# Performance work log

Measured on AMD Instinct MI355X. Metric: run time of the kernel, lower is better.

## Reference

```python
import jax, jax.numpy as jnp
import numpy as np

NH, NP = 8, 4  # n_heads, n_points
SHAPES = [(100, 167), (50, 84), (25, 42), (13, 21)]  # (H, W) per level


def setup_inputs() -> dict:
    key = jax.random.key(0)
    ks = jax.random.split(key, 8)
    bs, dm = 2, 256
    nl = len(SHAPES)
    nv = sum(h * w for h, w in SHAPES)  # 22223
    nq = nv
    s = 1.0 / np.sqrt(dm)
    return {
        'query': jax.random.normal(ks[0], (bs, nq, dm), jnp.float32),
        'value': jax.random.normal(ks[1], (bs, nv, dm), jnp.float32),
        'reference_points': jax.random.uniform(ks[2], (bs, nq, nl, 2), jnp.float32),
        'W_so': jax.random.normal(ks[3], (dm, NH * nl * NP * 2), jnp.float32) * 0.01,
        'b_so': jax.random.normal(ks[4], (NH * nl * NP * 2,), jnp.float32) * 0.5,
        'W_aw': jax.random.normal(ks[5], (dm, NH * nl * NP), jnp.float32) * s,
        'b_aw': jnp.zeros((NH * nl * NP,), jnp.float32),
        'W_vp': jax.random.normal(ks[6], (dm, dm), jnp.float32) * s,
        'b_vp': jnp.zeros((dm,), jnp.float32),
        'W_op': jax.random.normal(ks[7], (dm, dm), jnp.float32) * s,
        'b_op': jnp.zeros((dm,), jnp.float32),
        'spatial_shapes': jnp.array(SHAPES, jnp.int32),
    }


def _bilinear_gather(vf, H, W, loc):
    # vf: [BH, H*W, dh] flattened level feature map; loc: [BH, QP, 2] in [0,1]
    # Matches torch grid_sample(mode='bilinear', padding_mode='zeros', align_corners=False)
    x = loc[..., 0] * W - 0.5
    y = loc[..., 1] * H - 0.5
    x0f = jnp.floor(x); y0f = jnp.floor(y)
    lx = x - x0f; ly = y - y0f
    x0 = x0f.astype(jnp.int32); y0 = y0f.astype(jnp.int32)
    out = jnp.zeros(vf.shape[:1] + loc.shape[1:2] + vf.shape[-1:], vf.dtype)
    for dx, dy, w in ((0, 0, (1 - lx) * (1 - ly)), (1, 0, lx * (1 - ly)),
                      (0, 1, (1 - lx) * ly), (1, 1, lx * ly)):
        xi = x0 + dx; yi = y0 + dy
        valid = (xi >= 0) & (xi < W) & (yi >= 0) & (yi < H)
        idx = jnp.clip(yi, 0, H - 1) * W + jnp.clip(xi, 0, W - 1)  # [BH, QP]
        g = jnp.take_along_axis(vf, idx[:, :, None], axis=1)  # [BH, QP, dh]
        out = out + g * (w * valid)[:, :, None]
    return out


def _msda(value_heads, shapes_np, loc, aw):
    # value_heads: [bs,nv,nh,dh], loc: [bs,nq,nh,nl,np,2], aw: [bs,nq,nh,nl,np]
    bs, nv, nh, dh = value_heads.shape
    nq, nl, npnt = loc.shape[1], loc.shape[3], loc.shape[4]
    out = jnp.zeros((bs * nh, nq, dh), value_heads.dtype)
    start = 0
    for lvl in range(nl):
        H, W = int(shapes_np[lvl, 0]), int(shapes_np[lvl, 1])
        vf = value_heads[:, start:start + H * W].transpose(0, 2, 1, 3).reshape(bs * nh, H * W, dh)
        loc_l = loc[:, :, :, lvl].transpose(0, 2, 1, 3, 4).reshape(bs * nh, nq * npnt, 2)
        samp = _bilinear_gather(vf, H, W, loc_l).reshape(bs * nh, nq, npnt, dh)
        aw_l = aw[:, :, :, lvl].transpose(0, 2, 1, 3).reshape(bs * nh, nq, npnt)
        out = out + jnp.einsum('bqpd,bqp->bqd', samp, aw_l)
        start += H * W
    return out.reshape(bs, nh, nq, dh).transpose(0, 2, 1, 3).reshape(bs, nq, nh * dh)


def reference(query, value, reference_points, W_so, b_so, W_aw, b_aw, W_vp, b_vp, W_op, b_op, spatial_shapes):
    bs, nq, dm = query.shape
    nl = reference_points.shape[2]
    dh = dm // NH
    v = (value @ W_vp + b_vp).reshape(bs, value.shape[1], NH, dh)
    off = (query @ W_so + b_so).reshape(bs, nq, NH, nl, NP, 2)
    aw = jax.nn.softmax((query @ W_aw + b_aw).reshape(bs, nq, NH, nl * NP), axis=-1)
    aw = aw.reshape(bs, nq, NH, nl, NP)
    ss = np.asarray(spatial_shapes)  # static level metadata
    normalizer = jnp.asarray(np.stack([ss[:, 1], ss[:, 0]], -1), query.dtype)  # (w, h) per level
    loc = reference_points[:, :, None, :, None, :] + off / normalizer[None, None, None, :, None, :]
    out = _msda(v, ss, loc, aw)
    return out @ W_op + b_op + query  # identity residual (identity defaults to query)
```

## Files before the change

kernel.cpp:

```cpp
#include <hip/hip_runtime.h>
#include <hip/hip_bf16.h>
#include <math.h>

typedef __hip_bfloat16 bf16;
using f32x4  = __attribute__((ext_vector_type(4))) float;
using f32x2  = __attribute__((ext_vector_type(2))) float;
using bf16x8 = __attribute__((ext_vector_type(8))) short;
using f16x2  = __attribute__((ext_vector_type(2))) _Float16;

constexpr int BS = 2, NQ = 22223, MROWS = 44446;
constexpr int LH[4] = {100, 50, 25, 13};
constexpr int LW[4] = {167, 84, 42, 21};
constexpr int LSTART[4] = {0, 16700, 20900, 21950};
constexpr int PLW[4] = {170, 87, 45, 24};
constexpr int PLSTART[4] = {0, 17510, 22121, 23381};
constexpr int PTOT = 23765;

constexpr int BM = 128, BK = 32;
constexpr int LDT = 40;
constexpr int GX = (MROWS + BM - 1) / BM;

__global__ __launch_bounds__(256) void prep_weights(
    const float* __restrict__ W_vp, const float* __restrict__ W_so,
    const float* __restrict__ W_aw, const float* __restrict__ W_op,
    const float* __restrict__ b_so, const float* __restrict__ b_aw,
    bf16* __restrict__ Wt_vp, bf16* __restrict__ Wt_cat,
    bf16* __restrict__ Wt_op, float* __restrict__ bcat)
{
    int i = blockIdx.x * 256 + threadIdx.x;
    if (i < 256 * 256) {
        int n = i >> 8, k = i & 255;
        Wt_vp[i] = __float2bfloat16(W_vp[k * 256 + n]);
        Wt_op[i] = __float2bfloat16(W_op[k * 256 + n]);
    }
    if (i < 384 * 256) {
        int n = i >> 8, k = i & 255;
        float v = (n < 256) ? W_so[k * 256 + n] : W_aw[k * 128 + (n - 256)];
        Wt_cat[i] = __float2bfloat16(v);
    }
    if (i < 384) bcat[i] = (i < 256) ? b_so[i] : b_aw[i - 256];
}

__device__ inline int pad_base_idx(int pix) {
    if (pix < LSTART[1])      { int y = pix / 167;                  int x = pix - y * 167;                return PLSTART[0] + (y + 1) * 170 + (x + 1); }
    else if (pix < LSTART[2]) { int rel = pix - LSTART[1]; int y = rel / 84; int x = rel - y * 84;        return PLSTART[1] + (y + 1) * 87  + (x + 1); }
    else if (pix < LSTART[3]) { int rel = pix - LSTART[2]; int y = rel / 42; int x = rel - y * 42;        return PLSTART[2] + (y + 1) * 45  + (x + 1); }
    else                      { int rel = pix - LSTART[3]; int y = rel / 21; int x = rel - y * 21;        return PLSTART[3] + (y + 1) * 24  + (x + 1); }
}

template<bool A_BF16>
__device__ __forceinline__ void mfma_core(
    const void* __restrict__ Av, int lda, const bf16* __restrict__ Wt,
    int row0, int bn0, int M, bf16* As, bf16* Bs, f32x4 (&acc)[4][4])
{
    const int tid = threadIdx.x;
    const int lane = tid & 63;
    const int wv = tid >> 6;
    const int wm = (wv >> 1) * 64, wn = (wv & 1) * 64;
    const int l15 = lane & 15, l4 = lane >> 4;

#pragma unroll
    for (int m = 0; m < 4; ++m)
#pragma unroll
        for (int n = 0; n < 4; ++n) { acc[m][n][0]=0.f; acc[m][n][1]=0.f; acc[m][n][2]=0.f; acc[m][n][3]=0.f; }

    for (int k0 = 0; k0 < 256; k0 += BK) {
        __syncthreads();
#pragma unroll
        for (int t = 0; t < 2; ++t) {
            int idx = tid + t * 256;
            int r = idx >> 2, s = idx & 3;
            {
                int grow = row0 + r; if (grow >= M) grow = M - 1;
                bf16 tmp[8];
                if constexpr (A_BF16) {
                    const bf16* ap = (const bf16*)Av + (size_t)grow * lda + (k0 + s * 8);
                    *(uint4*)tmp = *(const uint4*)ap;
                } else {
                    const float* ap = (const float*)Av + (size_t)grow * lda + (k0 + s * 8);
                    f32x4 v0 = *(const f32x4*)ap;
                    f32x4 v1 = *(const f32x4*)(ap + 4);
#pragma unroll
                    for (int j = 0; j < 4; ++j) tmp[j] = __float2bfloat16(v0[j]);
#pragma unroll
                    for (int j = 0; j < 4; ++j) tmp[4 + j] = __float2bfloat16(v1[j]);
                }
                *(uint4*)&As[r * LDT + s * 8] = *(const uint4*)tmp;
            }
            *(uint4*)&Bs[r * LDT + s * 8] =
                *(const uint4*)(Wt + (size_t)(bn0 + r) * 256 + (k0 + s * 8));
        }
        __syncthreads();

        bf16x8 af[4], bfr[4];
#pragma unroll
        for (int m = 0; m < 4; ++m)
            af[m] = *(const bf16x8*)&As[(wm + m * 16 + l15) * LDT + l4 * 8];
#pragma unroll
        for (int n = 0; n < 4; ++n)
            bfr[n] = *(const bf16x8*)&Bs[(wn + n * 16 + l15) * LDT + l4 * 8];
#pragma unroll
        for (int m = 0; m < 4; ++m)
#pragma unroll
            for (int n = 0; n < 4; ++n)
                acc[m][n] = __builtin_amdgcn_mfma_f32_16x16x32_bf16(af[m], bfr[n], acc[m][n], 0, 0, 0);
    }
}

__global__ __launch_bounds__(256) void gemm_producer(
    const float* __restrict__ query, const float* __restrict__ value,
    const bf16* __restrict__ Wt_cat, const bf16* __restrict__ Wt_vp,
    const float* __restrict__ bcat, const float* __restrict__ bvp,
    bf16* __restrict__ offawl, _Float16* __restrict__ vproj)
{
    __shared__ bf16 As[BM * LDT];
    __shared__ bf16 Bs[BM * LDT];

    constexpr int NWG = GX * 5;
    constexpr int QXW = NWG / 8, RXW = NWG % 8;
    int orig = blockIdx.x;
    int xcd = orig & 7, seq = orig >> 3;
    int swz = (xcd < RXW ? xcd * (QXW + 1) : RXW * (QXW + 1) + (xcd - RXW) * QXW) + seq;
    int slice = swz % 5;
    int row0 = (swz / 5) * BM;

    const bool isOff = slice < 3;
    const void* A = isOff ? (const void*)query : (const void*)value;
    const bf16* Wt = isOff ? Wt_cat : Wt_vp;
    const float* bias = isOff ? bcat : bvp;
    int bn0 = isOff ? slice * 128 : (slice - 3) * 128;

    f32x4 acc[4][4];
    mfma_core<false>(A, 256, Wt, row0, bn0, MROWS, As, Bs, acc);

    const int lane = threadIdx.x & 63;
    const int wv = threadIdx.x >> 6;
    const int wm = (wv >> 1) * 64, wn = (wv & 1) * 64;
    const int l15 = lane & 15, l4 = lane >> 4;

    if (isOff) {
#pragma unroll
        for (int m = 0; m < 4; ++m)
#pragma unroll
            for (int j = 0; j < 4; ++j) {
                int r = row0 + wm + m * 16 + l4 * 4 + j;
                if (r < MROWS) {
                    bf16* orow = offawl + (size_t)r * 384;
#pragma unroll
                    for (int n = 0; n < 4; ++n) {
                        int fcol = bn0 + wn + n * 16 + l15;
                        orow[fcol] = __float2bfloat16(acc[m][n][j] + bias[fcol]);
                    }
                }
            }
    } else {
#pragma unroll
        for (int m = 0; m < 4; ++m)
#pragma unroll
            for (int j = 0; j < 4; ++j) {
                int r = row0 + wm + m * 16 + l4 * 4 + j;
                if (r < MROWS) {
                    int bb = (r >= NQ) ? 1 : 0;
                    int pb = pad_base_idx(r - bb * NQ);
#pragma unroll
                    for (int n = 0; n < 4; ++n) {
                        int fcol = bn0 + wn + n * 16 + l15;
                        int hh = fcol >> 5, cc = fcol & 31;
                        vproj[((size_t)(hh * 2 + bb) * PTOT + pb) * 32 + cc] =
                            (_Float16)(acc[m][n][j] + bias[fcol]);
                    }
                }
            }
    }
}

__global__ __launch_bounds__(256) void gemm_out(
    const bf16* __restrict__ msda, const bf16* __restrict__ Wt_op,
    const float* __restrict__ b_op, const float* __restrict__ query,
    float* __restrict__ out)
{
    __shared__ bf16 As[BM * LDT];
    __shared__ bf16 Bs[BM * LDT];

    constexpr int NWG = GX * 2;
    int orig = blockIdx.x;
    int swz = (orig & 7) * (NWG / 8) + (orig >> 3);
    int bn0 = (swz & 1) * 128;
    int row0 = (swz >> 1) * BM;

    f32x4 acc[4][4];
    mfma_core<true>(msda, 384, Wt_op, row0, bn0, MROWS, As, Bs, acc);

    const int lane = threadIdx.x & 63;
    const int wv = threadIdx.x >> 6;
    const int wm = (wv >> 1) * 64, wn = (wv & 1) * 64;
    const int l15 = lane & 15, l4 = lane >> 4;

#pragma unroll
    for (int m = 0; m < 4; ++m)
#pragma unroll
        for (int j = 0; j < 4; ++j) {
            int r = row0 + wm + m * 16 + l4 * 4 + j;
            if (r < MROWS) {
#pragma unroll
                for (int n = 0; n < 4; ++n) {
                    int fcol = bn0 + wn + n * 16 + l15;
                    out[(size_t)r * 256 + fcol] =
                        acc[m][n][j] + b_op[fcol] + query[(size_t)r * 256 + fcol];
                }
            }
        }
}

__device__ inline f32x2 bfpair(unsigned u) {
    f32x2 r;
    r.x = __uint_as_float(u << 16);
    r.y = __uint_as_float(u & 0xffff0000u);
    return r;
}

__global__ __launch_bounds__(256)
__attribute__((amdgpu_waves_per_eu(2, 4)))
void msda_sample18(
    const _Float16* __restrict__ vproj,
    const bf16* __restrict__ offawl,
    const float* __restrict__ refp,
    bf16* __restrict__ msda_out)
{
    __shared__ uint2 sOff[32][8];
    __shared__ uint2 sAwl[32][4];
    __shared__ float sRef[32][8];

    const int tid = threadIdx.x;
    const int head = blockIdx.x & 7;
    const int qbase = (blockIdx.x >> 3) * 32;

    {
        int row = tid >> 3, e = tid & 7;
        int grow = min(qbase + row, MROWS - 1);
        sOff[row][e] = *((const uint2*)(offawl + (size_t)grow * 384 + head * 32) + e);
        sRef[row][e] = refp[(size_t)grow * 8 + e];
        if (tid < 128) {
            int rowa = tid >> 2, ea = tid & 3;
            int growa = min(qbase + rowa, MROWS - 1);
            sAwl[rowa][ea] = *((const uint2*)(offawl + (size_t)growa * 384 + 256 + head * 16) + ea);
        }
    }
    __syncthreads();

    const int w = tid >> 6;
    const int lane = tid & 63;
    const int ql = lane >> 3;
    const int s = lane & 7;
    const int sx = s >> 2;
    const int c16 = s & 3;
    const int lq = w * 8 + ql;
    int q = qbase + lq;
    const bool alive = q < MROWS;
    if (!alive) q = MROWS - 1;
    const int b = (q >= NQ) ? 1 : 0;

    float aw0, aw1;
    {
        unsigned lgu = ((const unsigned*)&sAwl[lq][0])[s];
        f32x2 lg = bfpair(lgu);
        float m = fmaxf(lg.x, lg.y);
        m = fmaxf(m, __shfl_xor(m, 1));
        m = fmaxf(m, __shfl_xor(m, 2));
        m = fmaxf(m, __shfl_xor(m, 4));
        float e0 = __expf(lg.x - m), e1 = __expf(lg.y - m);
        float ssum = e0 + e1;
        ssum += __shfl_xor(ssum, 1);
        ssum += __shfl_xor(ssum, 2);
        ssum += __shfl_xor(ssum, 4);
        float inv = 1.f / ssum;
        aw0 = e0 * inv;
        aw1 = e1 * inv;
    }

    int rpix0, rpix1;
    int rw00, rw10, rw01, rw11;
    {
        const int lo = s >> 1;
        const int Wl  = (lo == 0) ? 167 : (lo == 1) ? 84 : (lo == 2) ? 42 : 21;
        const int Hl  = (lo == 0) ? 100 : (lo == 1) ? 50 : (lo == 2) ? 25 : 13;
        const int Wpl = (lo == 0) ? 170 : (lo == 1) ? 87 : (lo == 2) ? 45 : 24;
        const float xb = sRef[lq][lo * 2 + 0] * (float)Wl + 0.5f;
        const float yb = sRef[lq][lo * 2 + 1] * (float)Hl + 0.5f;
        uint2 ou = sOff[lq][s];
        unsigned ouv[2] = {ou.x, ou.y};
        float awv[2] = {aw0, aw1};
        int pixv[2]; int w0v[2], w1v[2];
#pragma unroll
        for (int k = 0; k < 2; ++k) {
            f32x2 o2 = bfpair(ouv[k]);
            float x = fminf(fmaxf(xb + o2.x, 0.f), (float)(Wl + 1));
            float y = fminf(fmaxf(yb + o2.y, 0.f), (float)(Hl + 1));
            float x0f = floorf(x), y0f = floorf(y);
            float lx = x - x0f, ly = y - y0f;
            float a = awv[k];
            float wy0 = (1.f - ly) * a, wy1 = ly * a;
            float wx0 = 1.f - lx;
            pixv[k] = ((int)y0f * Wpl + (int)x0f) * 32;
            w0v[k] = (int)__builtin_bit_cast(unsigned,
                        f16x2{(_Float16)(wx0 * wy0), (_Float16)(wx0 * wy1)});
            w1v[k] = (int)__builtin_bit_cast(unsigned,
                        f16x2{(_Float16)(lx * wy0), (_Float16)(lx * wy1)});
        }
        rpix0 = pixv[0]; rw00 = w0v[0]; rw10 = w1v[0];
        rpix1 = pixv[1]; rw01 = w0v[1]; rw11 = w1v[1];
    }

    const int srcbase = lane & 56;
    f16x2 acc0 = {0, 0}, acc1 = {0, 0}, acc2 = {0, 0}, acc3 = {0, 0};

#pragma unroll
    for (int l = 0; l < 4; ++l) {
        const int Wp = PLW[l];
        const _Float16* vl = vproj + ((size_t)(head * 2 + b) * PTOT + PLSTART[l]) * 32
                             + sx * 32 + c16 * 8;

        const _Float16* pr[4][2];
        f16x2 hw0[4], hw1[4];
#pragma unroll
        for (int p = 0; p < 4; ++p) {
            const int t = l * 4 + p;
            const int src = srcbase | (t >> 1);
            int pix, wa, wb;
            if (t & 1) {
                pix = __shfl(rpix1, src);
                wa  = __shfl(rw01, src);
                wb  = __shfl(rw11, src);
            } else {
                pix = __shfl(rpix0, src);
                wa  = __shfl(rw00, src);
                wb  = __shfl(rw10, src);
            }
            f16x2 wv = __builtin_bit_cast(f16x2, (unsigned)(sx ? wb : wa));
            hw0[p] = f16x2{wv[0], wv[0]};
            hw1[p] = f16x2{wv[1], wv[1]};
            pr[p][0] = vl + pix;
            pr[p][1] = pr[p][0] + Wp * 32;
        }

        uint4 c[4][2];
#pragma unroll
        for (int p = 0; p < 4; ++p) {
            c[p][0] = *(const uint4*)pr[p][0];
            c[p][1] = *(const uint4*)pr[p][1];
        }

#pragma unroll
        for (int p = 0; p < 4; ++p) {
            acc0 += __builtin_bit_cast(f16x2, c[p][0].x) * hw0[p];
            acc1 += __builtin_bit_cast(f16x2, c[p][0].y) * hw0[p];
            acc2 += __builtin_bit_cast(f16x2, c[p][0].z) * hw0[p];
            acc3 += __builtin_bit_cast(f16x2, c[p][0].w) * hw0[p];
            acc0 += __builtin_bit_cast(f16x2, c[p][1].x) * hw1[p];
            acc1 += __builtin_bit_cast(f16x2, c[p][1].y) * hw1[p];
            acc2 += __builtin_bit_cast(f16x2, c[p][1].z) * hw1[p];
            acc3 += __builtin_bit_cast(f16x2, c[p][1].w) * hw1[p];
        }
    }

    {
        unsigned u0 = __builtin_bit_cast(unsigned, acc0);
        unsigned u1 = __builtin_bit_cast(unsigned, acc1);
        unsigned u2 = __builtin_bit_cast(unsigned, acc2);
        unsigned u3 = __builtin_bit_cast(unsigned, acc3);
        acc0 += __builtin_bit_cast(f16x2, __shfl_xor((int)u0, 4));
        acc1 += __builtin_bit_cast(f16x2, __shfl_xor((int)u1, 4));
        acc2 += __builtin_bit_cast(f16x2, __shfl_xor((int)u2, 4));
        acc3 += __builtin_bit_cast(f16x2, __shfl_xor((int)u3, 4));
    }

    if (alive && sx == 0) {
        bf16 ob[8];
        ob[0] = __float2bfloat16((float)acc0[0]);
        ob[1] = __float2bfloat16((float)acc0[1]);
        ob[2] = __float2bfloat16((float)acc1[0]);
        ob[3] = __float2bfloat16((float)acc1[1]);
        ob[4] = __float2bfloat16((float)acc2[0]);
        ob[5] = __float2bfloat16((float)acc2[1]);
        ob[6] = __float2bfloat16((float)acc3[0]);
        ob[7] = __float2bfloat16((float)acc3[1]);
        *(uint4*)(msda_out + (size_t)q * 384 + head * 32 + c16 * 8) = *(const uint4*)ob;
    }
}

extern "C" void kernel_launch(void* const* d_in, const int* in_sizes, int n_in,
                              void* d_out, int out_size, void* d_ws, size_t ws_size,
                              hipStream_t stream) {
    const float* query = (const float*)d_in[0];
    const float* value = (const float*)d_in[1];
    const float* refp  = (const float*)d_in[2];
    const float* W_so  = (const float*)d_in[3];
    const float* b_so  = (const float*)d_in[4];
    const float* W_aw  = (const float*)d_in[5];
    const float* b_aw  = (const float*)d_in[6];
    const float* W_vp  = (const float*)d_in[7];
    const float* b_vp  = (const float*)d_in[8];
    const float* W_op  = (const float*)d_in[9];
    const float* b_op  = (const float*)d_in[10];
    float* out = (float*)d_out;

    bf16*     d_offawl = (bf16*)d_ws;
    _Float16* d_vproj  = (_Float16*)(d_offawl + (size_t)MROWS * 384);
    bf16*     d_wtcat  = (bf16*)(d_vproj + (size_t)16 * PTOT * 32);
    bf16*     d_wtvp   = d_wtcat + 384 * 256;
    bf16*     d_wtop   = d_wtvp + 256 * 256;
    float*    d_bcat   = (float*)(d_wtop + 256 * 256);

    prep_weights<<<384, 256, 0, stream>>>(W_vp, W_so, W_aw, W_op, b_so, b_aw,
                                          d_wtvp, d_wtcat, d_wtop, d_bcat);
    hipMemsetAsync(d_vproj, 0, (size_t)16 * PTOT * 32 * sizeof(_Float16), stream);

    gemm_producer<<<GX * 5, 256, 0, stream>>>(
        query, value, d_wtcat, d_wtvp, d_bcat, b_vp, d_offawl, d_vproj);

    msda_sample18<<<8 * ((MROWS + 31) / 32), 256, 0, stream>>>(
        d_vproj, d_offawl, refp, d_offawl);

    gemm_out<<<GX * 2, 256, 0, stream>>>(d_offawl, d_wtop, b_op, query, out);
}
```

Before: 138.4 us.

## Load GEMM operands directly from global into registers, dropping LDS staging

Both GEMM kernels stop staging A and B tiles through shared memory with barriers. Each wave now loads its MFMA fragments straight from global memory, and the K loop is fully unrolled. This removes the LDS round trip and the __syncthreads calls, and lets loads be issued ahead of the MFMAs. The cost is that data shared between waves is no longer reused in LDS, so global and L2 traffic per workgroup roughly doubles, and the fully unrolled loop raises register pressure.

```diff
diff --git a/kernel.cpp b/kernel.cpp
--- a/kernel.cpp
+++ b/kernel.cpp
@@ -16,8 +16,7 @@
 constexpr int PLSTART[4] = {0, 17510, 22121, 23381};
 constexpr int PTOT = 23765;
 
-constexpr int BM = 128, BK = 32;
-constexpr int LDT = 40;
+constexpr int BM = 128;
 constexpr int GX = (MROWS + BM - 1) / BM;
 
 __global__ __launch_bounds__(256) void prep_weights(
@@ -49,56 +48,55 @@
 }
 
 template<bool A_BF16>
-__device__ __forceinline__ void mfma_core(
+__device__ __forceinline__ void mfma_direct(
     const void* __restrict__ Av, int lda, const bf16* __restrict__ Wt,
-    int row0, int bn0, int M, bf16* As, bf16* Bs, f32x4 (&acc)[4][4])
+    int row0, int bn0, int M, f32x4 (&acc)[4][4])
 {
-    const int tid = threadIdx.x;
-    const int lane = tid & 63;
-    const int wv = tid >> 6;
+    const int lane = threadIdx.x & 63;
+    const int wv = threadIdx.x >> 6;
     const int wm = (wv >> 1) * 64, wn = (wv & 1) * 64;
     const int l15 = lane & 15, l4 = lane >> 4;
 
+    int arow[4];
+#pragma unroll
+    for (int m = 0; m < 4; ++m) {
+        int r = row0 + wm + m * 16 + l15;
+        arow[m] = (r < M) ? r : (M - 1);
+    }
+    const bf16* brow[4];
+#pragma unroll
+    for (int n = 0; n < 4; ++n)
+        brow[n] = Wt + (size_t)(bn0 + wn + n * 16 + l15) * 256 + l4 * 8;
+
 #pragma unroll
     for (int m = 0; m < 4; ++m)
 #pragma unroll
         for (int n = 0; n < 4; ++n) { acc[m][n][0]=0.f; acc[m][n][1]=0.f; acc[m][n][2]=0.f; acc[m][n][3]=0.f; }
 
-    for (int k0 = 0; k0 < 256; k0 += BK) {
-        __syncthreads();
-#pragma unroll
-        for (int t = 0; t < 2; ++t) {
-            int idx = tid + t * 256;
-            int r = idx >> 2, s = idx & 3;
-            {
-                int grow = row0 + r; if (grow >= M) grow = M - 1;
+#pragma unroll
+    for (int k0 = 0; k0 < 256; k0 += 32) {
+        bf16x8 af[4], bfr[4];
+#pragma unroll
+        for (int m = 0; m < 4; ++m) {
+            if constexpr (A_BF16) {
+                const bf16* ap = (const bf16*)Av + (size_t)arow[m] * lda + k0 + l4 * 8;
+                af[m] = *(const bf16x8*)ap;
+            } else {
+                const float* ap = (const float*)Av + (size_t)arow[m] * lda + k0 + l4 * 8;
+                f32x4 v0 = *(const f32x4*)ap;
+                f32x4 v1 = *(const f32x4*)(ap + 4);
                 bf16 tmp[8];
-                if constexpr (A_BF16) {
-                    const bf16* ap = (const bf16*)Av + (size_t)grow * lda + (k0 + s * 8);
-                    *(uint4*)tmp = *(const uint4*)ap;
-                } else {
-                    const float* ap = (const float*)Av + (size_t)grow * lda + (k0 + s * 8);
-                    f32x4 v0 = *(const f32x4*)ap;
-                    f32x4 v1 = *(const f32x4*)(ap + 4);
-#pragma unroll
-                    for (int j = 0; j < 4; ++j) tmp[j] = __float2bfloat16(v0[j]);
-#pragma unroll
-                    for (int j = 0; j < 4; ++j) tmp[4 + j] = __float2bfloat16(v1[j]);
-                }
-                *(uint4*)&As[r * LDT + s * 8] = *(const uint4*)tmp;
+#pragma unroll
+                for (int j = 0; j < 4; ++j) tmp[j] = __float2bfloat16(v0[j]);
+#pragma unroll
+                for (int j = 0; j < 4; ++j) tmp[4 + j] = __float2bfloat16(v1[j]);
+                af[m] = *(const bf16x8*)tmp;
             }
-            *(uint4*)&Bs[r * LDT + s * 8] =
-                *(const uint4*)(Wt + (size_t)(bn0 + r) * 256 + (k0 + s * 8));
-        }
-        __syncthreads();
-
-        bf16x8 af[4], bfr[4];
-#pragma unroll
-        for (int m = 0; m < 4; ++m)
-            af[m] = *(const bf16x8*)&As[(wm + m * 16 + l15) * LDT + l4 * 8];
+        }
 #pragma unroll
         for (int n = 0; n < 4; ++n)
-            bfr[n] = *(const bf16x8*)&Bs[(wn + n * 16 + l15) * LDT + l4 * 8];
+            bfr[n] = *(const bf16x8*)(brow[n] + k0);
+
 #pragma unroll
         for (int m = 0; m < 4; ++m)
 #pragma unroll
@@ -113,9 +111,6 @@
     const float* __restrict__ bcat, const float* __restrict__ bvp,
     bf16* __restrict__ offawl, _Float16* __restrict__ vproj)
 {
-    __shared__ bf16 As[BM * LDT];
-    __shared__ bf16 Bs[BM * LDT];
-
     constexpr int NWG = GX * 5;
     constexpr int QXW = NWG / 8, RXW = NWG % 8;
     int orig = blockIdx.x;
@@ -131,7 +126,7 @@
     int bn0 = isOff ? slice * 128 : (slice - 3) * 128;
 
     f32x4 acc[4][4];
-    mfma_core<false>(A, 256, Wt, row0, bn0, MROWS, As, Bs, acc);
+    mfma_direct<false>(A, 256, Wt, row0, bn0, MROWS, acc);
 
     const int lane = threadIdx.x & 63;
     const int wv = threadIdx.x >> 6;
@@ -179,9 +174,6 @@
     const float* __restrict__ b_op, const float* __restrict__ query,
     float* __restrict__ out)
 {
-    __shared__ bf16 As[BM * LDT];
-    __shared__ bf16 Bs[BM * LDT];
-
     constexpr int NWG = GX * 2;
     int orig = blockIdx.x;
     int swz = (orig & 7) * (NWG / 8) + (orig >> 3);
@@ -189,7 +181,7 @@
     int row0 = (swz >> 1) * BM;
 
     f32x4 acc[4][4];
-    mfma_core<true>(msda, 384, Wt_op, row0, bn0, MROWS, As, Bs, acc);
+    mfma_direct<true>(msda, 384, Wt_op, row0, bn0, MROWS, acc);
 
     const int lane = threadIdx.x & 63;
     const int wv = threadIdx.x >> 6;
```

New measurement: 204.0 us. 47.4% more time.

## Double-buffer LDS tiles and prefetch next K-slice in GEMM core

Applied to the files above, without the earlier changes.

Replaces the single-buffered GEMM main loop with a double-buffered version. The next K-slice of A and B is loaded from global memory into registers before the current slice's MFMAs run, then written to the alternate LDS buffer. This removes one barrier per iteration and hides global load latency behind compute. In exchange it doubles LDS use per block and adds register pressure, which can lower occupancy.

```diff
diff --git a/kernel.cpp b/kernel.cpp
--- a/kernel.cpp
+++ b/kernel.cpp
@@ -16,7 +16,7 @@
 constexpr int PLSTART[4] = {0, 17510, 22121, 23381};
 constexpr int PTOT = 23765;
 
-constexpr int BM = 128, BK = 32;
+constexpr int BM = 128;
 constexpr int LDT = 40;
 constexpr int GX = (MROWS + BM - 1) / BM;
 
@@ -49,7 +49,7 @@
 }
 
 template<bool A_BF16>
-__device__ __forceinline__ void mfma_core(
+__device__ __forceinline__ void mfma_core_db(
     const void* __restrict__ Av, int lda, const bf16* __restrict__ Wt,
     int row0, int bn0, int M, bf16* As, bf16* Bs, f32x4 (&acc)[4][4])
 {
@@ -59,51 +59,69 @@
     const int wm = (wv >> 1) * 64, wn = (wv & 1) * 64;
     const int l15 = lane & 15, l4 = lane >> 4;
 
+    const int sr0 = tid >> 2;
+    const int sr1 = sr0 + 64;
+    const int ss = tid & 3;
+    const int ga0 = min(row0 + sr0, M - 1);
+    const int ga1 = min(row0 + sr1, M - 1);
+
 #pragma unroll
     for (int m = 0; m < 4; ++m)
 #pragma unroll
         for (int n = 0; n < 4; ++n) { acc[m][n][0]=0.f; acc[m][n][1]=0.f; acc[m][n][2]=0.f; acc[m][n][3]=0.f; }
 
-    for (int k0 = 0; k0 < 256; k0 += BK) {
+    bf16 tA0[8], tA1[8];
+    uint4 tB0, tB1;
+
+    auto load_regs = [&](int k0) {
+        if constexpr (A_BF16) {
+            *(uint4*)tA0 = *(const uint4*)((const bf16*)Av + (size_t)ga0 * lda + k0 + ss * 8);
+            *(uint4*)tA1 = *(const uint4*)((const bf16*)Av + (size_t)ga1 * lda + k0 + ss * 8);
+        } else {
+            const float* ap0 = (const float*)Av + (size_t)ga0 * lda + k0 + ss * 8;
+            const float* ap1 = (const float*)Av + (size_t)ga1 * lda + k0 + ss * 8;
+            f32x4 v0 = *(const f32x4*)ap0, v1 = *(const f32x4*)(ap0 + 4);
+            f32x4 u0 = *(const f32x4*)ap1, u1 = *(const f32x4*)(ap1 + 4);
+#pragma unroll
+            for (int j = 0; j < 4; ++j) { tA0[j] = __float2bfloat16(v0[j]); tA0[4+j] = __float2bfloat16(v1[j]); }
+#pragma unroll
+            for (int j = 0; j < 4; ++j) { tA1[j] = __float2bfloat16(u0[j]); tA1[4+j] = __float2bfloat16(u1[j]); }
+        }
+        tB0 = *(const uint4*)(Wt + (size_t)(bn0 + sr0) * 256 + k0 + ss * 8);
+        tB1 = *(const uint4*)(Wt + (size_t)(bn0 + sr1) * 256 + k0 + ss * 8);
+    };
+    auto write_lds = [&](bf16* A_, bf16* B_) {
+        *(uint4*)&A_[sr0 * LDT + ss * 8] = *(const uint4*)tA0;
+        *(uint4*)&A_[sr1 * LDT + ss * 8] = *(const uint4*)tA1;
+        *(uint4*)&B_[sr0 * LDT + ss * 8] = tB0;
+        *(uint4*)&B_[sr1 * LDT + ss * 8] = tB1;
+    };
+
+    load_regs(0);
+    write_lds(As, Bs);
+    bf16 *curA = As, *curB = Bs;
+    bf16 *nxtA = As + BM * LDT, *nxtB = Bs + BM * LDT;
+
+#pragma unroll
+    for (int k = 0; k < 8; ++k) {
+        if (k < 7) load_regs((k + 1) * 32);
         __syncthreads();
-#pragma unroll
-        for (int t = 0; t < 2; ++t) {
-            int idx = tid + t * 256;
-            int r = idx >> 2, s = idx & 3;
-            {
-                int grow = row0 + r; if (grow >= M) grow = M - 1;
-                bf16 tmp[8];
-                if constexpr (A_BF16) {
-                    const bf16* ap = (const bf16*)Av + (size_t)grow * lda + (k0 + s * 8);
-                    *(uint4*)tmp = *(const uint4*)ap;
-                } else {
-                    const float* ap = (const float*)Av + (size_t)grow * lda + (k0 + s * 8);
-                    f32x4 v0 = *(const f32x4*)ap;
-                    f32x4 v1 = *(const f32x4*)(ap + 4);
-#pragma unroll
-                    for (int j = 0; j < 4; ++j) tmp[j] = __float2bfloat16(v0[j]);
-#pragma unroll
-                    for (int j = 0; j < 4; ++j) tmp[4 + j] = __float2bfloat16(v1[j]);
-                }
-                *(uint4*)&As[r * LDT + s * 8] = *(const uint4*)tmp;
-            }
-            *(uint4*)&Bs[r * LDT + s * 8] =
-                *(const uint4*)(Wt + (size_t)(bn0 + r) * 256 + (k0 + s * 8));
-        }
-        __syncthreads();
-
         bf16x8 af[4], bfr[4];
 #pragma unroll
         for (int m = 0; m < 4; ++m)
-            af[m] = *(const bf16x8*)&As[(wm + m * 16 + l15) * LDT + l4 * 8];
+            af[m] = *(const bf16x8*)&curA[(wm + m * 16 + l15) * LDT + l4 * 8];
 #pragma unroll
         for (int n = 0; n < 4; ++n)
-            bfr[n] = *(const bf16x8*)&Bs[(wn + n * 16 + l15) * LDT + l4 * 8];
+            bfr[n] = *(const bf16x8*)&curB[(wn + n * 16 + l15) * LDT + l4 * 8];
+        if (k < 7) write_lds(nxtA, nxtB);
 #pragma unroll
         for (int m = 0; m < 4; ++m)
 #pragma unroll
             for (int n = 0; n < 4; ++n)
                 acc[m][n] = __builtin_amdgcn_mfma_f32_16x16x32_bf16(af[m], bfr[n], acc[m][n], 0, 0, 0);
+        bf16* t;
+        t = curA; curA = nxtA; nxtA = t;
+        t = curB; curB = nxtB; nxtB = t;
     }
 }
 
@@ -113,8 +131,8 @@
     const float* __restrict__ bcat, const float* __restrict__ bvp,
     bf16* __restrict__ offawl, _Float16* __restrict__ vproj)
 {
-    __shared__ bf16 As[BM * LDT];
-    __shared__ bf16 Bs[BM * LDT];
+    __shared__ bf16 As[2 * BM * LDT];
+    __shared__ bf16 Bs[2 * BM * LDT];
 
     constexpr int NWG = GX * 5;
     constexpr int QXW = NWG / 8, RXW = NWG % 8;
@@ -131,7 +149,7 @@
     int bn0 = isOff ? slice * 128 : (slice - 3) * 128;
 
     f32x4 acc[4][4];
-    mfma_core<false>(A, 256, Wt, row0, bn0, MROWS, As, Bs, acc);
+    mfma_core_db<false>(A, 256, Wt, row0, bn0, MROWS, As, Bs, acc);
 
     const int lane = threadIdx.x & 63;
     const int wv = threadIdx.x >> 6;
@@ -179,8 +197,8 @@
     const float* __restrict__ b_op, const float* __restrict__ query,
     float* __restrict__ out)
 {
-    __shared__ bf16 As[BM * LDT];
-    __shared__ bf16 Bs[BM * LDT];
+    __shared__ bf16 As[2 * BM * LDT];
+    __shared__ bf16 Bs[2 * BM * LDT];
 
     constexpr int NWG = GX * 2;
     int orig = blockIdx.x;
@@ -189,7 +207,7 @@
     int row0 = (swz >> 1) * BM;
 
     f32x4 acc[4][4];
-    mfma_core<true>(msda, 384, Wt_op, row0, bn0, MROWS, As, Bs, acc);
+    mfma_core_db<true>(msda, 384, Wt_op, row0, bn0, MROWS, As, Bs, acc);
 
     const int lane = threadIdx.x & 63;
     const int wv = threadIdx.x >> 6;
```

After: 139.6 us. No clear change (+0.9%).
